# Performance work log

Measured on AMD Instinct MI355X. Metric: run time of the kernel, lower is better.

Reference implementation:

```python
import jax, jax.numpy as jnp
import numpy as np

RANK = 8
LN_EPS = 1e-5


def setup_inputs() -> dict:
    key = jax.random.key(0)
    ks = jax.random.split(key, 8)
    B, T, D = 16, 1024, 1024
    A = 1024          # ada_dim
    I = 1024          # inter_dim
    OUT = D * RANK * 4  # 32768
    s = 0.02
    return {
        "x": jax.random.normal(ks[0], (B, T, D), jnp.float32),
        "ada_emb": jax.random.normal(ks[1], (B, A), jnp.float32),
        "base_up": jax.random.normal(ks[2], (D, D), jnp.float32) * s,
        "base_down": jax.random.normal(ks[3], (D, D), jnp.float32) * s,
        "ln_gamma": jnp.ones((A,), jnp.float32),
        "ln_beta": jnp.zeros((A,), jnp.float32),
        "W1": jax.random.normal(ks[4], (A, I), jnp.float32) / np.sqrt(A),
        "bias1": jnp.zeros((I,), jnp.float32),
        "W2": jax.random.normal(ks[5], (I, OUT), jnp.float32) / np.sqrt(I),
        "bias2": jnp.zeros((OUT,), jnp.float32),
    }


def reference(x, ada_emb, base_up, base_down, ln_gamma, ln_beta, W1, bias1, W2, bias2):
    B, T, D = x.shape
    R = RANK
    # norm_cond: LayerNorm over ada_dim (biased variance, eps=1e-5)
    mu = jnp.mean(ada_emb, axis=-1, keepdims=True)
    var = jnp.mean(jnp.square(ada_emb - mu), axis=-1, keepdims=True)
    c = (ada_emb - mu) / jnp.sqrt(var + LN_EPS) * ln_gamma + ln_beta
    # gen_weight: Linear -> GELU -> Linear
    h = jax.nn.gelu(c @ W1 + bias1, approximate=False)
    w = h @ W2 + bias2                         # (B, 4*D*R)
    a1, b1, a2, b2 = [t.reshape(B, D, R) for t in jnp.split(w, 4, axis=-1)]
    # down matvec: x @ (base_down + a2 @ b2^T), factored to avoid (B,D,D)
    u = jnp.einsum('btd,bdr->btr', x, a2)      # (B,T,R)
    mid = jnp.einsum('btd,dl->btl', x, base_down) + jnp.einsum('btr,blr->btl', u, b2)
    mid = jax.nn.gelu(mid, approximate=False)  # act_fn between layers
    # up matvec: (base_up + a1 @ b1^T) @ mid, factored
    v = jnp.einsum('blr,btl->btr', b1, mid)    # (B,T,R)
    out = jnp.einsum('btl,kl->btk', mid, base_up) + jnp.einsum('bkr,btr->btk', a1, v)
    return x + out  # residual
```

## Files before the change

### kernel.cpp

```cpp
#include <hip/hip_runtime.h>
#include <math.h>

#define DD 1024
#define NB 16
#define WSPLIT 4
#define HSPLIT 32

typedef unsigned short u16;
typedef __attribute__((ext_vector_type(8))) short short8;
typedef __attribute__((ext_vector_type(4))) float f32x4;
typedef __attribute__((ext_vector_type(16))) float f32x16;

__device__ __forceinline__ float gelu_f(float x) {
  return 0.5f * x * (1.0f + erff(x * 0.70710678118654752440f));
}
__device__ __forceinline__ u16 f2bf(float f) {
  union { float f; unsigned u; } v; v.f = f;
  return (u16)((v.u + 0x7FFFu + ((v.u >> 16) & 1u)) >> 16);
}
__device__ __forceinline__ float bf2f(u16 b) {
  union { unsigned u; float f; } v; v.u = ((unsigned)b) << 16;
  return v.f;
}
__device__ __forceinline__ void gload_lds16(const u16* g, u16* l) {
  __builtin_amdgcn_global_load_lds(
      (const __attribute__((address_space(1))) void*)g,
      (__attribute__((address_space(3))) void*)l, 16, 0, 0);
}
__device__ __forceinline__ void gload_lds16f(const float* g, float* l) {
  __builtin_amdgcn_global_load_lds(
      (const __attribute__((address_space(1))) void*)g,
      (__attribute__((address_space(3))) void*)l, 16, 0, 0);
}

#define VMCNT8   asm volatile("s_waitcnt vmcnt(8)" ::: "memory")
#define VMCNT4   asm volatile("s_waitcnt vmcnt(4)" ::: "memory")
#define VMCNT0   asm volatile("s_waitcnt vmcnt(0)" ::: "memory")
#define BARRIER  asm volatile("s_barrier" ::: "memory")

__launch_bounds__(256)
__global__ void prep_kernel(const float* __restrict__ x, u16* __restrict__ xb,
                            const float* __restrict__ ada, const float* __restrict__ gamma,
                            const float* __restrict__ beta, float* __restrict__ c,
                            const float* __restrict__ bdn, u16* __restrict__ bdTb,
                            const float* __restrict__ bu, u16* __restrict__ bub) {
  __shared__ float smem[1056];
  int bid = blockIdx.x;
  int t = threadIdx.x;
  if (bid < 8192) {
    size_t i = (size_t)bid * 256 + t;
    const float4* xf = (const float4*)x;
    float4 v0 = xf[i * 2], v1 = xf[i * 2 + 1];
    short8 o;
    o[0] = (short)f2bf(v0.x); o[1] = (short)f2bf(v0.y);
    o[2] = (short)f2bf(v0.z); o[3] = (short)f2bf(v0.w);
    o[4] = (short)f2bf(v1.x); o[5] = (short)f2bf(v1.y);
    o[6] = (short)f2bf(v1.z); o[7] = (short)f2bf(v1.w);
    *(short8*)(xb + i * 8) = o;
  } else if (bid < 8208) {
    int b = bid - 8192;
    const float* row = ada + b * DD;
    float s = 0.f, s2 = 0.f;
    for (int i = t; i < DD; i += 256) { float v = row[i]; s += v; s2 += v * v; }
    for (int off = 32; off; off >>= 1) { s += __shfl_down(s, off); s2 += __shfl_down(s2, off); }
    float* rs = smem; float* rs2 = smem + 4;
    int wave = t >> 6, lane = t & 63;
    if (lane == 0) { rs[wave] = s; rs2[wave] = s2; }
    __syncthreads();
    if (t == 0) {
      float a = 0.f, a2 = 0.f;
      for (int w = 0; w < 4; w++) { a += rs[w]; a2 += rs2[w]; }
      rs[0] = a * (1.0f / DD); rs2[0] = a2 * (1.0f / DD);
    }
    __syncthreads();
    float mu = rs[0];
    float var = rs2[0] - mu * mu;
    float inv = rsqrtf(var + 1e-5f);
    for (int i = t; i < DD; i += 256)
      c[b * DD + i] = (row[i] - mu) * inv * gamma[i] + beta[i];
  } else if (bid < 9232) {
    int t2 = bid - 8208;
    int bx = (t2 & 31) * 32, by = (t2 >> 5) * 32;
    float (*tile)[33] = (float(*)[33])smem;
    int tx = t & 31, ty = t >> 5;
    for (int r = ty; r < 32; r += 8) tile[r][tx] = bdn[(size_t)(by + r) * DD + bx + tx];
    __syncthreads();
    for (int r = ty; r < 32; r += 8)
      bdTb[(size_t)(bx + r) * DD + by + tx] = f2bf(tile[tx][r]);
  } else {
    size_t i = (size_t)(bid - 9232) * 256 + t;
    const float4* bf = (const float4*)bu;
    float4 v0 = bf[i * 2], v1 = bf[i * 2 + 1];
    short8 o;
    o[0] = (short)f2bf(v0.x); o[1] = (short)f2bf(v0.y);
    o[2] = (short)f2bf(v0.z); o[3] = (short)f2bf(v0.w);
    o[4] = (short)f2bf(v1.x); o[5] = (short)f2bf(v1.y);
    o[6] = (short)f2bf(v1.z); o[7] = (short)f2bf(v1.w);
    *(short8*)(bub + i * 8) = o;
  }
}

__launch_bounds__(256)
__global__ void h_part_kernel(const float* __restrict__ c, const float* __restrict__ W1,
                              float* __restrict__ hpart) {
  int s = blockIdx.y;
  int j = blockIdx.x * 256 + threadIdx.x;
  int k0 = s * 32;
  __shared__ float cs[NB][32];
  for (int i = threadIdx.x; i < NB * 32; i += 256)
    cs[i >> 5][i & 31] = c[(size_t)(i >> 5) * DD + k0 + (i & 31)];
  __syncthreads();
  float acc[NB];
  #pragma unroll
  for (int b = 0; b < NB; b++) acc[b] = 0.f;
  #pragma unroll
  for (int al = 0; al < 32; al++) {
    float wv = W1[(size_t)(k0 + al) * DD + j];
    #pragma unroll
    for (int b = 0; b < NB; b++) acc[b] += cs[b][al] * wv;
  }
  #pragma unroll
  for (int b = 0; b < NB; b++)
    hpart[((size_t)s * NB + b) * DD + j] = acc[b];
}

__launch_bounds__(256)
__global__ void h_reduce_kernel(const float* __restrict__ hpart, const float* __restrict__ bias1,
                                float* __restrict__ h) {
  int idx = blockIdx.x * 256 + threadIdx.x;
  int j = idx & (DD - 1);
  float acc = bias1[j];
  #pragma unroll
  for (int s = 0; s < HSPLIT; s++) acc += hpart[(size_t)s * NB * DD + idx];
  h[idx] = gelu_f(acc);
}

#define WSTAGE(ST, BUF) do { int kr_ = k0 + (ST) * 16;                                      \
    _Pragma("unroll")                                                                       \
    for (int i_ = 0; i_ < 4; i_++)                                                          \
      gload_lds16f(W2 + (size_t)(kr_ + i_ * 4 + (t >> 6)) * 32768 + j0 + ((t & 63) << 2),   \
                   &wlds[BUF][i_ * 4 + (t >> 6)][(t & 63) << 2]);                           \
  } while (0)

__launch_bounds__(256)
__global__ void w_part_kernel(const float* __restrict__ h, const float* __restrict__ W2,
                              float* __restrict__ part) {
  int s = blockIdx.y;
  int j0 = blockIdx.x * 256;
  int k0 = s * 256;
  int t = threadIdx.x;
  __shared__ __align__(16) float wlds[2][16][256];
  __shared__ __align__(16) float hlT[256][20];

  #pragma unroll
  for (int v = 0; v < 16; v++) {
    int i = t + v * 256;
    hlT[i & 255][i >> 8] = h[(size_t)(i >> 8) * DD + k0 + (i & 255)];
  }

  WSTAGE(0, 0);
  WSTAGE(1, 1);

  float acc[NB] = {};

  #pragma unroll 1
  for (int st = 0; st < 16; st++) {
    if (st < 15) { VMCNT4; } else { VMCNT0; }
    BARRIER;
    int buf = st & 1;
    #pragma unroll
    for (int r = 0; r < 16; r++) {
      float wv = wlds[buf][r][t];
      int kk = st * 16 + r;
      f32x4 h0 = *(const f32x4*)&hlT[kk][0];
      f32x4 h1 = *(const f32x4*)&hlT[kk][4];
      f32x4 h2 = *(const f32x4*)&hlT[kk][8];
      f32x4 h3 = *(const f32x4*)&hlT[kk][12];
      #pragma unroll
      for (int q = 0; q < 4; q++) {
        acc[q]      += h0[q] * wv;
        acc[q + 4]  += h1[q] * wv;
        acc[q + 8]  += h2[q] * wv;
        acc[q + 12] += h3[q] * wv;
      }
    }
    BARRIER;
    if (st + 2 < 16) WSTAGE(st + 2, buf);
  }

  #pragma unroll
  for (int b = 0; b < NB; b++)
    part[((size_t)s * NB + b) * 32768 + j0 + t] = acc[b];
}

__launch_bounds__(256)
__global__ void w_reduce_kernel(const float* __restrict__ part, const float* __restrict__ bias2,
                                float* __restrict__ w) {
  int idx = blockIdx.x * 256 + threadIdx.x;
  int j = idx & 32767;
  float acc = bias2[j];
  #pragma unroll
  for (int s = 0; s < WSPLIT; s++) acc += part[(size_t)s * NB * 32768 + idx];
  w[idx] = acc;
}

__launch_bounds__(256)
__global__ void pack_lora_kernel(const u16* __restrict__ src, const float* __restrict__ w,
                                 int aoff, int boff,
                                 u16* __restrict__ aext, u16* __restrict__ bext) {
  int b = blockIdx.y;
  const float* wb = w + (size_t)b * 32768;
  int t = threadIdx.x;
  short8 z = {};
  if (blockIdx.x < 16) {
    __shared__ float a2s[8192];
    for (int i = t; i < 8192; i += 256) a2s[i] = wb[aoff + i];
    __syncthreads();
    int row = blockIdx.x * 64 + (t >> 2);
    int q = t & 3;
    const u16* xr = src + ((size_t)b << 20) + (size_t)row * DD + q * 256;
    float acc[8] = {};
    #pragma unroll 4
    for (int kk = 0; kk < 32; kk++) {
      short8 xv = *(const short8*)(xr + kk * 8);
      #pragma unroll
      for (int e = 0; e < 8; e++) {
        float xf = bf2f((u16)xv[e]);
        int d = q * 256 + kk * 8 + e;
        #pragma unroll
        for (int r = 0; r < 8; r++) acc[r] += xf * a2s[d * 8 + r];
      }
    }
    #pragma unroll
    for (int r = 0; r < 8; r++) {
      acc[r] += __shfl_xor(acc[r], 1);
      acc[r] += __shfl_xor(acc[r], 2);
    }
    short8 ov = z;
    if (q == 0) {
      #pragma unroll
      for (int r = 0; r < 8; r++) ov[r] = (short)f2bf(acc[r]);
    }
    u16* orow = aext + ((size_t)b * 1024 + row) * 64 + q * 16;
    *(short8*)orow = ov;
    *(short8*)(orow + 8) = z;
  } else {
    for (int l = t; l < 1024; l += 256) {
      short8 ov;
      #pragma unroll
      for (int r = 0; r < 8; r++) ov[r] = (short)f2bf(wb[boff + l * 8 + r]);
      u16* orow = bext + ((size_t)b * 1024 + l) * 64;
      *(short8*)orow = ov;
      #pragma unroll
      for (int k = 1; k < 8; k++) *(short8*)(orow + k * 8) = z;
    }
  }
}

#define STAGE_A(KT, BUF) do { int kt_ = (KT);                                          \
    if (kt_ < 16) { int ks_ = kt_ * 64;                                                \
      _Pragma("unroll")                                                                \
      for (int c_ = 0; c_ < 4; c_++)                                                   \
        gload_lds16(Ab + (size_t)srow[c_] * DD + ks_ + se[c_], As[BUF] + ldsel[c_]);   \
    } else {                                                                           \
      _Pragma("unroll")                                                                \
      for (int c_ = 0; c_ < 4; c_++)                                                   \
        gload_lds16(Ae + (size_t)srow[c_] * 64 + se[c_], As[BUF] + ldsel[c_]);         \
    } } while (0)
#define STAGE_B(KT, BUF) do { int kt_ = (KT);                                          \
    if (kt_ < 16) { int ks_ = kt_ * 64;                                                \
      _Pragma("unroll")                                                                \
      for (int c_ = 0; c_ < 4; c_++)                                                   \
        gload_lds16(Bb + (size_t)srow[c_] * DD + ks_ + se[c_], Bs[BUF] + ldsel[c_]);   \
    } else {                                                                           \
      _Pragma("unroll")                                                                \
      for (int c_ = 0; c_ < 4; c_++)                                                   \
        gload_lds16(Be + (size_t)srow[c_] * 64 + se[c_], Bs[BUF] + ldsel[c_]);         \
    } } while (0)

template<int PHASE>
__launch_bounds__(512, 2)
__global__ void gemm256_kernel(const u16* __restrict__ A, const u16* __restrict__ BT,
                               const u16* __restrict__ Aext, const u16* __restrict__ Bext,
                               const u16* __restrict__ resid, void* __restrict__ Cout) {
  constexpr int BK = 64;
  constexpr int NT = 17;
  __shared__ __align__(16) u16 As[2][256 * BK];
  __shared__ __align__(16) u16 Bs[2][256 * BK];

  int orig = blockIdx.x;
  int logical = (orig & 7) * 32 + (orig >> 3);
  int b = logical >> 4;
  int tile = logical & 15;
  int tm = tile >> 2, tn = tile & 3;

  const u16* Ab = A + ((size_t)b << 20) + (size_t)(tm * 256) * DD;
  const u16* Bb = BT + (size_t)(tn * 256) * DD;
  const u16* Ae = Aext + ((size_t)b * 1024 + tm * 256) * 64;
  const u16* Be = Bext + ((size_t)b * 1024 + tn * 256) * 64;

  int t = threadIdx.x, lane = t & 63;
  int l31 = lane & 31, kb = (lane >> 5) * 8;
  int wave = t >> 6;
  int wm = wave >> 2, wn = wave & 3;

  int srow[4], se[4], ldsel[4];
  #pragma unroll
  for (int c = 0; c < 4; c++) {
    int chunk = c * 512 + t;
    srow[c] = chunk >> 3;
    se[c] = ((chunk & 7) ^ (srow[c] & 7)) << 3;
    ldsel[c] = chunk * 8;
  }

  f32x16 acc[4][2] = {};

  STAGE_A(0, 0); STAGE_B(0, 0);
  STAGE_A(1, 1); STAGE_B(1, 1);
  VMCNT8;
  BARRIER;

  int cur = 0;
  #pragma unroll 1
  for (int kt = 0; kt < NT; kt++) {
    const u16* Ap = As[cur];
    const u16* Bp = Bs[cur];
    short8 afr[2][4], bf0[4], bf1[4];

    #pragma unroll
    for (int ks = 0; ks < 4; ks++) {
      #pragma unroll
      for (int rt = 0; rt < 2; rt++) {
        int r = wm * 128 + rt * 32 + l31;
        int e = (ks * 16 + kb) ^ ((r & 7) << 3);
        afr[rt][ks] = *(const short8*)(Ap + r * BK + e);
      }
      {
        int r = wn * 64 + l31;
        int e = (ks * 16 + kb) ^ ((r & 7) << 3);
        bf0[ks] = *(const short8*)(Bp + r * BK + e);
      }
    }
    __builtin_amdgcn_s_setprio(1);
    #pragma unroll
    for (int ks = 0; ks < 4; ks++)
      #pragma unroll
      for (int rt = 0; rt < 2; rt++)
        acc[rt][0] = __builtin_amdgcn_mfma_f32_32x32x16_bf16(afr[rt][ks], bf0[ks], acc[rt][0], 0, 0, 0);
    __builtin_amdgcn_s_setprio(0);

    #pragma unroll
    for (int ks = 0; ks < 4; ks++) {
      int r = wn * 64 + 32 + l31;
      int e = (ks * 16 + kb) ^ ((r & 7) << 3);
      bf1[ks] = *(const short8*)(Bp + r * BK + e);
    }
    __builtin_amdgcn_s_setprio(1);
    #pragma unroll
    for (int ks = 0; ks < 4; ks++)
      #pragma unroll
      for (int rt = 0; rt < 2; rt++)
        acc[rt][1] = __builtin_amdgcn_mfma_f32_32x32x16_bf16(afr[rt][ks], bf1[ks], acc[rt][1], 0, 0, 0);
    __builtin_amdgcn_s_setprio(0);

    #pragma unroll
    for (int ks = 0; ks < 4; ks++)
      #pragma unroll
      for (int rt = 0; rt < 2; rt++) {
        int r = wm * 128 + (rt + 2) * 32 + l31;
        int e = (ks * 16 + kb) ^ ((r & 7) << 3);
        afr[rt][ks] = *(const short8*)(Ap + r * BK + e);
      }
    __builtin_amdgcn_s_setprio(1);
    #pragma unroll
    for (int ks = 0; ks < 4; ks++)
      #pragma unroll
      for (int rt = 0; rt < 2; rt++)
        acc[rt + 2][1] = __builtin_amdgcn_mfma_f32_32x32x16_bf16(afr[rt][ks], bf1[ks], acc[rt + 2][1], 0, 0, 0);

    #pragma unroll
    for (int ks = 0; ks < 4; ks++)
      #pragma unroll
      for (int rt = 0; rt < 2; rt++)
        acc[rt + 2][0] = __builtin_amdgcn_mfma_f32_32x32x16_bf16(afr[rt][ks], bf0[ks], acc[rt + 2][0], 0, 0, 0);
    __builtin_amdgcn_s_setprio(0);

    BARRIER;
    if (kt + 2 < NT) {
      STAGE_B(kt + 2, cur);
      STAGE_A(kt + 2, cur);
      VMCNT8;
    } else {
      VMCNT0;
    }
    BARRIER;

    cur ^= 1;
  }

  int r0 = tm * 256 + wm * 128 + (lane >> 5) * 4;
  int c0 = tn * 256 + wn * 64 + l31;
  if (PHASE == 1) {
    u16* mid = (u16*)Cout + ((size_t)b << 20);
    #pragma unroll
    for (int rt = 0; rt < 4; rt++)
      #pragma unroll
      for (int ct = 0; ct < 2; ct++)
        #pragma unroll
        for (int reg = 0; reg < 16; reg++) {
          int row = r0 + rt * 32 + (reg & 3) + 8 * (reg >> 2);
          int col = c0 + ct * 32;
          mid[(size_t)row * DD + col] = f2bf(gelu_f(acc[rt][ct][reg]));
        }
  } else {
    float* out = (float*)Cout + ((size_t)b << 20);
    const u16* xb = resid + ((size_t)b << 20);
    #pragma unroll
    for (int rt = 0; rt < 4; rt++)
      #pragma unroll
      for (int ct = 0; ct < 2; ct++)
        #pragma unroll
        for (int reg = 0; reg < 16; reg++) {
          int row = r0 + rt * 32 + (reg & 3) + 8 * (reg >> 2);
          int col = c0 + ct * 32;
          size_t idx = (size_t)row * DD + col;
          out[idx] = bf2f(xb[idx]) + acc[rt][ct][reg];
        }
  }
}

extern "C" void kernel_launch(void* const* d_in, const int* in_sizes, int n_in,
                              void* d_out, int out_size, void* d_ws, size_t ws_size,
                              hipStream_t stream) {
  const float* x         = (const float*)d_in[0];
  const float* ada       = (const float*)d_in[1];
  const float* base_up   = (const float*)d_in[2];
  const float* base_down = (const float*)d_in[3];
  const float* gamma     = (const float*)d_in[4];
  const float* beta      = (const float*)d_in[5];
  const float* W1        = (const float*)d_in[6];
  const float* bias1     = (const float*)d_in[7];
  const float* W2        = (const float*)d_in[8];
  const float* bias2     = (const float*)d_in[9];
  float* out = (float*)d_out;
  char* ws = (char*)d_ws;

  float* c     = (float*)(ws);
  float* h     = (float*)(ws + 0x10000);
  float* w     = (float*)(ws + 0x20000);
  u16*   bdTb  = (u16*)  (ws + 0x220000);
  u16*   bub   = (u16*)  (ws + 0x420000);
  float* hpart = (float*)(ws + 0x620000);
  u16*   xb    = (u16*)  (ws + 0x820000);
  u16*   uext  = (u16*)  (ws + 0x2820000);
  u16*   b2ext = (u16*)  (ws + 0x2A20000);
  u16*   vext  = (u16*)  (ws + 0x2C20000);
  u16*   a1ext = (u16*)  (ws + 0x2E20000);
  u16*   mid   = (u16*)  (ws + 0x3020000);
  float* part  = (float*)(ws + 0x5020000);

  prep_kernel<<<dim3(9744), dim3(256), 0, stream>>>(x, xb, ada, gamma, beta, c,
                                                    base_down, bdTb, base_up, bub);
  h_part_kernel<<<dim3(4, HSPLIT), dim3(256), 0, stream>>>(c, W1, hpart);
  h_reduce_kernel<<<dim3(64), dim3(256), 0, stream>>>(hpart, bias1, h);
  w_part_kernel<<<dim3(128, WSPLIT), dim3(256), 0, stream>>>(h, W2, part);
  w_reduce_kernel<<<dim3(2048), dim3(256), 0, stream>>>(part, bias2, w);
  pack_lora_kernel<<<dim3(17, 16), dim3(256), 0, stream>>>(xb, w, 16384, 24576, uext, b2ext);
  gemm256_kernel<1><<<dim3(256), dim3(512), 0, stream>>>(xb, bdTb, uext, b2ext,
                                                         (const u16*)nullptr, (void*)mid);
  pack_lora_kernel<<<dim3(17, 16), dim3(256), 0, stream>>>(mid, w, 8192, 0, vext, a1ext);
  gemm256_kernel<2><<<dim3(256), dim3(512), 0, stream>>>(mid, bub, vext, a1ext, xb, (void*)out);
}
```

Baseline: 254.6 us.

## Switch GEMM to 16x16x32 MFMA tiles and fold w-reduce into pack kernel

```diff
diff --git a/kernel.cpp b/kernel.cpp
--- a/kernel.cpp
+++ b/kernel.cpp
@@ -9,7 +9,6 @@
 typedef unsigned short u16;
 typedef __attribute__((ext_vector_type(8))) short short8;
 typedef __attribute__((ext_vector_type(4))) float f32x4;
-typedef __attribute__((ext_vector_type(16))) float f32x16;
 
 __device__ __forceinline__ float gelu_f(float x) {
   return 0.5f * x * (1.0f + erff(x * 0.70710678118654752440f));
@@ -194,28 +193,22 @@
 }
 
 __launch_bounds__(256)
-__global__ void w_reduce_kernel(const float* __restrict__ part, const float* __restrict__ bias2,
-                                float* __restrict__ w) {
-  int idx = blockIdx.x * 256 + threadIdx.x;
-  int j = idx & 32767;
-  float acc = bias2[j];
-  #pragma unroll
-  for (int s = 0; s < WSPLIT; s++) acc += part[(size_t)s * NB * 32768 + idx];
-  w[idx] = acc;
-}
-
-__launch_bounds__(256)
-__global__ void pack_lora_kernel(const u16* __restrict__ src, const float* __restrict__ w,
-                                 int aoff, int boff,
+__global__ void pack_lora_kernel(const u16* __restrict__ src, const float* __restrict__ part,
+                                 const float* __restrict__ bias2, int aoff, int boff,
                                  u16* __restrict__ aext, u16* __restrict__ bext) {
   int b = blockIdx.y;
-  const float* wb = w + (size_t)b * 32768;
   int t = threadIdx.x;
+  int off = (blockIdx.x < 16) ? aoff : boff;
+  __shared__ float fac[8192];
+  for (int i = t; i < 8192; i += 256) {
+    float acc = bias2[off + i];
+    #pragma unroll
+    for (int s = 0; s < WSPLIT; s++) acc += part[((size_t)s * NB + b) * 32768 + off + i];
+    fac[i] = acc;
+  }
+  __syncthreads();
   short8 z = {};
   if (blockIdx.x < 16) {
-    __shared__ float a2s[8192];
-    for (int i = t; i < 8192; i += 256) a2s[i] = wb[aoff + i];
-    __syncthreads();
     int row = blockIdx.x * 64 + (t >> 2);
     int q = t & 3;
     const u16* xr = src + ((size_t)b << 20) + (size_t)row * DD + q * 256;
@@ -228,7 +221,7 @@
         float xf = bf2f((u16)xv[e]);
         int d = q * 256 + kk * 8 + e;
         #pragma unroll
-        for (int r = 0; r < 8; r++) acc[r] += xf * a2s[d * 8 + r];
+        for (int r = 0; r < 8; r++) acc[r] += xf * fac[d * 8 + r];
       }
     }
     #pragma unroll
@@ -248,7 +241,7 @@
     for (int l = t; l < 1024; l += 256) {
       short8 ov;
       #pragma unroll
-      for (int r = 0; r < 8; r++) ov[r] = (short)f2bf(wb[boff + l * 8 + r]);
+      for (int r = 0; r < 8; r++) ov[r] = (short)f2bf(fac[l * 8 + r]);
       u16* orow = bext + ((size_t)b * 1024 + l) * 64;
       *(short8*)orow = ov;
       #pragma unroll
@@ -299,8 +292,7 @@
   const u16* Ae = Aext + ((size_t)b * 1024 + tm * 256) * 64;
   const u16* Be = Bext + ((size_t)b * 1024 + tn * 256) * 64;
 
-  int t = threadIdx.x, lane = t & 63;
-  int l31 = lane & 31, kb = (lane >> 5) * 8;
+  int t = threadIdx.x, lane = t & 63, g = lane >> 4, l15 = lane & 15;
   int wave = t >> 6;
   int wm = wave >> 2, wn = wave & 3;
 
@@ -313,7 +305,7 @@
     ldsel[c] = chunk * 8;
   }
 
-  f32x16 acc[4][2] = {};
+  f32x4 acc[8][4] = {};
 
   STAGE_A(0, 0); STAGE_B(0, 0);
   STAGE_A(1, 1); STAGE_B(1, 1);
@@ -325,65 +317,30 @@
   for (int kt = 0; kt < NT; kt++) {
     const u16* Ap = As[cur];
     const u16* Bp = Bs[cur];
-    short8 afr[2][4], bf0[4], bf1[4];
-
-    #pragma unroll
-    for (int ks = 0; ks < 4; ks++) {
-      #pragma unroll
-      for (int rt = 0; rt < 2; rt++) {
-        int r = wm * 128 + rt * 32 + l31;
-        int e = (ks * 16 + kb) ^ ((r & 7) << 3);
-        afr[rt][ks] = *(const short8*)(Ap + r * BK + e);
+
+    #pragma unroll
+    for (int kk = 0; kk < 2; kk++) {
+      short8 af[8], bf[4];
+      #pragma unroll
+      for (int i = 0; i < 8; i++) {
+        int r = wm * 128 + i * 16 + l15;
+        int e = (kk * 32 + g * 8) ^ ((r & 7) << 3);
+        af[i] = *(const short8*)(Ap + r * BK + e);
       }
-      {
-        int r = wn * 64 + l31;
-        int e = (ks * 16 + kb) ^ ((r & 7) << 3);
-        bf0[ks] = *(const short8*)(Bp + r * BK + e);
+      #pragma unroll
+      for (int j = 0; j < 4; j++) {
+        int r = wn * 64 + j * 16 + l15;
+        int e = (kk * 32 + g * 8) ^ ((r & 7) << 3);
+        bf[j] = *(const short8*)(Bp + r * BK + e);
       }
-    }
-    __builtin_amdgcn_s_setprio(1);
-    #pragma unroll
-    for (int ks = 0; ks < 4; ks++)
-      #pragma unroll
-      for (int rt = 0; rt < 2; rt++)
-        acc[rt][0] = __builtin_amdgcn_mfma_f32_32x32x16_bf16(afr[rt][ks], bf0[ks], acc[rt][0], 0, 0, 0);
-    __builtin_amdgcn_s_setprio(0);
-
-    #pragma unroll
-    for (int ks = 0; ks < 4; ks++) {
-      int r = wn * 64 + 32 + l31;
-      int e = (ks * 16 + kb) ^ ((r & 7) << 3);
-      bf1[ks] = *(const short8*)(Bp + r * BK + e);
-    }
-    __builtin_amdgcn_s_setprio(1);
-    #pragma unroll
-    for (int ks = 0; ks < 4; ks++)
-      #pragma unroll
-      for (int rt = 0; rt < 2; rt++)
-        acc[rt][1] = __builtin_amdgcn_mfma_f32_32x32x16_bf16(afr[rt][ks], bf1[ks], acc[rt][1], 0, 0, 0);
-    __builtin_amdgcn_s_setprio(0);
-
-    #pragma unroll
-    for (int ks = 0; ks < 4; ks++)
-      #pragma unroll
-      for (int rt = 0; rt < 2; rt++) {
-        int r = wm * 128 + (rt + 2) * 32 + l31;
-        int e = (ks * 16 + kb) ^ ((r & 7) << 3);
-        afr[rt][ks] = *(const short8*)(Ap + r * BK + e);
-      }
-    __builtin_amdgcn_s_setprio(1);
-    #pragma unroll
-    for (int ks = 0; ks < 4; ks++)
-      #pragma unroll
-      for (int rt = 0; rt < 2; rt++)
-        acc[rt + 2][1] = __builtin_amdgcn_mfma_f32_32x32x16_bf16(afr[rt][ks], bf1[ks], acc[rt + 2][1], 0, 0, 0);
-
-    #pragma unroll
-    for (int ks = 0; ks < 4; ks++)
-      #pragma unroll
-      for (int rt = 0; rt < 2; rt++)
-        acc[rt + 2][0] = __builtin_amdgcn_mfma_f32_32x32x16_bf16(afr[rt][ks], bf0[ks], acc[rt + 2][0], 0, 0, 0);
-    __builtin_amdgcn_s_setprio(0);
+      __builtin_amdgcn_s_setprio(1);
+      #pragma unroll
+      for (int i = 0; i < 8; i++)
+        #pragma unroll
+        for (int j = 0; j < 4; j++)
+          acc[i][j] = __builtin_amdgcn_mfma_f32_16x16x32_bf16(af[i], bf[j], acc[i][j], 0, 0, 0);
+      __builtin_amdgcn_s_setprio(0);
+    }
 
     BARRIER;
     if (kt + 2 < NT) {
@@ -398,33 +355,32 @@
     cur ^= 1;
   }
 
-  int r0 = tm * 256 + wm * 128 + (lane >> 5) * 4;
-  int c0 = tn * 256 + wn * 64 + l31;
+  int r0 = tm * 256 + wm * 128, c0 = tn * 256 + wn * 64;
   if (PHASE == 1) {
     u16* mid = (u16*)Cout + ((size_t)b << 20);
     #pragma unroll
-    for (int rt = 0; rt < 4; rt++)
-      #pragma unroll
-      for (int ct = 0; ct < 2; ct++)
+    for (int i = 0; i < 8; i++)
+      #pragma unroll
+      for (int j = 0; j < 4; j++)
         #pragma unroll
-        for (int reg = 0; reg < 16; reg++) {
-          int row = r0 + rt * 32 + (reg & 3) + 8 * (reg >> 2);
-          int col = c0 + ct * 32;
-          mid[(size_t)row * DD + col] = f2bf(gelu_f(acc[rt][ct][reg]));
+        for (int r = 0; r < 4; r++) {
+          int row = r0 + i * 16 + g * 4 + r;
+          int col = c0 + j * 16 + l15;
+          mid[(size_t)row * DD + col] = f2bf(gelu_f(acc[i][j][r]));
         }
   } else {
     float* out = (float*)Cout + ((size_t)b << 20);
     const u16* xb = resid + ((size_t)b << 20);
     #pragma unroll
-    for (int rt = 0; rt < 4; rt++)
-      #pragma unroll
-      for (int ct = 0; ct < 2; ct++)
+    for (int i = 0; i < 8; i++)
+      #pragma unroll
+      for (int j = 0; j < 4; j++)
         #pragma unroll
-        for (int reg = 0; reg < 16; reg++) {
-          int row = r0 + rt * 32 + (reg & 3) + 8 * (reg >> 2);
-          int col = c0 + ct * 32;
+        for (int r = 0; r < 4; r++) {
+          int row = r0 + i * 16 + g * 4 + r;
+          int col = c0 + j * 16 + l15;
           size_t idx = (size_t)row * DD + col;
-          out[idx] = bf2f(xb[idx]) + acc[rt][ct][reg];
+          out[idx] = bf2f(xb[idx]) + acc[i][j][r];
         }
   }
 }
@@ -447,7 +403,6 @@
 
   float* c     = (float*)(ws);
   float* h     = (float*)(ws + 0x10000);
-  float* w     = (float*)(ws + 0x20000);
   u16*   bdTb  = (u16*)  (ws + 0x220000);
   u16*   bub   = (u16*)  (ws + 0x420000);
   float* hpart = (float*)(ws + 0x620000);
@@ -464,10 +419,11 @@
   h_part_kernel<<<dim3(4, HSPLIT), dim3(256), 0, stream>>>(c, W1, hpart);
   h_reduce_kernel<<<dim3(64), dim3(256), 0, stream>>>(hpart, bias1, h);
   w_part_kernel<<<dim3(128, WSPLIT), dim3(256), 0, stream>>>(h, W2, part);
-  w_reduce_kernel<<<dim3(2048), dim3(256), 0, stream>>>(part, bias2, w);
-  pack_lora_kernel<<<dim3(17, 16), dim3(256), 0, stream>>>(xb, w, 16384, 24576, uext, b2ext);
+  pack_lora_kernel<<<dim3(17, 16), dim3(256), 0, stream>>>(xb, part, bias2, 16384, 24576,
+                                                           uext, b2ext);
   gemm256_kernel<1><<<dim3(256), dim3(512), 0, stream>>>(xb, bdTb, uext, b2ext,
                                                          (const u16*)nullptr, (void*)mid);
-  pack_lora_kernel<<<dim3(17, 16), dim3(256), 0, stream>>>(mid, w, 8192, 0, vext, a1ext);
+  pack_lora_kernel<<<dim3(17, 16), dim3(256), 0, stream>>>(mid, part, bias2, 8192, 0,
+                                                           vext, a1ext);
   gemm256_kernel<2><<<dim3(256), dim3(512), 0, stream>>>(mid, bub, vext, a1ext, xb, (void*)out);
 }
```

New measurement: 256.3 us. About the same (+0.7%).
